# Optimization experiments

Hardware: AMD Instinct MI355X
Metric: run time of the kernel (lower is better)

## Reference

```python
import jax, jax.numpy as jnp
import numpy as np

DIM = 1536; FFN = 8960; NH = 12; HD = DIM // NH
B = 1; Fg, Hg, Wg = 8, 20, 20; L = Fg * Hg * Wg; L2 = 512
EPS = 1e-6; MAXLEN = 1024


def _rope_tables():
    # Wan rope_params: per-axis inverse-frequency tables, concatenated [t|h|w]
    c = HD // 2; c0 = c - 2 * (c // 3); c1 = c // 3
    def ang(dp):
        inv = 1.0 / (10000.0 ** (np.arange(0, dp, 2, dtype=np.float64) / dp))
        return np.outer(np.arange(MAXLEN, dtype=np.float64), inv)
    a = np.concatenate([ang(2 * c0), ang(2 * c1), ang(2 * c1)], axis=1)  # [1024, c]
    return np.cos(a).astype(np.float32), np.sin(a).astype(np.float32)


def setup_inputs() -> dict:
    key = jax.random.key(0)
    ks = jax.random.split(key, 32); it = iter(range(32))
    def rnd(shape, scale=0.02):
        return jax.random.normal(ks[next(it)], shape, dtype=jnp.float32) * scale
    cos, sin = _rope_tables()
    inp = {
        'x': rnd((B, L, DIM), 1.0),
        'e': rnd((B, 6, DIM), 1.0),
        'context': rnd((B, L2, DIM), 1.0),
        'freqs_cos': jnp.asarray(cos), 'freqs_sin': jnp.asarray(sin),
        'modulation': rnd((1, 6, DIM), DIM ** -0.5),
    }
    for p in ['sa', 'ca']:
        for nm in ['q', 'k', 'v', 'o']:
            inp[p + '_' + nm + 'w'] = rnd((DIM, DIM))
            inp[p + '_' + nm + 'b'] = jnp.zeros((DIM,), jnp.float32)
        inp[p + '_nq'] = jnp.ones((DIM,), jnp.float32)
        inp[p + '_nk'] = jnp.ones((DIM,), jnp.float32)
    inp['n3_w'] = jnp.ones((DIM,), jnp.float32); inp['n3_b'] = jnp.zeros((DIM,), jnp.float32)
    inp['ffn_w1'] = rnd((DIM, FFN)); inp['ffn_b1'] = jnp.zeros((FFN,), jnp.float32)
    inp['ffn_w2'] = rnd((FFN, DIM)); inp['ffn_b2'] = jnp.zeros((DIM,), jnp.float32)
    inp['grid_f'] = Fg; inp['grid_h'] = Hg; inp['grid_w'] = Wg
    return inp


def _layer_norm(x, w=None, b=None):
    mu = x.mean(-1, keepdims=True)
    var = jnp.mean((x - mu) ** 2, -1, keepdims=True)
    y = (x - mu) * jax.lax.rsqrt(var + EPS)
    return y * w + b if w is not None else y


def _rms(x, w):
    return x * jax.lax.rsqrt(jnp.mean(x * x, -1, keepdims=True) + EPS) * w


def _rope(xq, cos, sin, f, h, w):
    # xq: [B, L, n, d]; complex rotation per (t,h,w) axis with split freq dims
    b, s, n, d = xq.shape
    c = d // 2; c0 = c - 2 * (c // 3); c1 = c // 3
    def grid(tab):
        t = jnp.broadcast_to(tab[:f, None, None, :c0], (f, h, w, c0))
        hh = jnp.broadcast_to(tab[None, :h, None, c0:c0 + c1], (f, h, w, c1))
        ww = jnp.broadcast_to(tab[None, None, :w, c0 + c1:c0 + 2 * c1], (f, h, w, c1))
        return jnp.concatenate([t, hh, ww], -1).reshape(f * h * w, c)
    gc = grid(cos)[None, :, None, :]  # [1, L, 1, c]
    gs = grid(sin)[None, :, None, :]
    xr = xq.reshape(b, s, n, c, 2)
    xre, xim = xr[..., 0], xr[..., 1]
    return jnp.stack([xre * gc - xim * gs, xre * gs + xim * gc], -1).reshape(b, s, n, d)


def _attn(q, k, v):
    scores = jnp.einsum('bqnd,bknd->bnqk', q, k) * (q.shape[-1] ** -0.5)
    p = jax.nn.softmax(scores, -1)
    return jnp.einsum('bnqk,bknd->bqnd', p, v)


def reference(x, e, context, freqs_cos, freqs_sin, modulation,
              sa_qw, sa_qb, sa_kw, sa_kb, sa_vw, sa_vb, sa_ow, sa_ob, sa_nq, sa_nk,
              ca_qw, ca_qb, ca_kw, ca_kb, ca_vw, ca_vb, ca_ow, ca_ob, ca_nq, ca_nk,
              n3_w, n3_b, ffn_w1, ffn_b1, ffn_w2, ffn_b2,
              grid_f, grid_h, grid_w):
    b, s, _ = x.shape; n, d = NH, HD
    em = modulation + e  # [B, 6, C]
    e0, e1, e2, e3, e4, e5 = (em[:, i:i + 1] for i in range(6))
    # self-attention with adaLN modulation
    xs = _layer_norm(x) * (1 + e1) + e0
    q = _rms(xs @ sa_qw + sa_qb, sa_nq).reshape(b, s, n, d)
    k = _rms(xs @ sa_kw + sa_kb, sa_nk).reshape(b, s, n, d)
    v = (xs @ sa_vw + sa_vb).reshape(b, s, n, d)
    q = _rope(q, freqs_cos, freqs_sin, grid_f, grid_h, grid_w)
    k = _rope(k, freqs_cos, freqs_sin, grid_f, grid_h, grid_w)
    y = _attn(q, k, v).reshape(b, s, -1) @ sa_ow + sa_ob
    x = x + y * e2
    # cross-attention on norm3(x)
    xc = _layer_norm(x, n3_w, n3_b)
    s2 = context.shape[1]
    cq = _rms(xc @ ca_qw + ca_qb, ca_nq).reshape(b, s, n, d)
    ck = _rms(context @ ca_kw + ca_kb, ca_nk).reshape(b, s2, n, d)
    cv = (context @ ca_vw + ca_vb).reshape(b, s2, n, d)
    x = x + (_attn(cq, ck, cv).reshape(b, s, -1) @ ca_ow + ca_ob)
    # FFN with adaLN modulation
    xf = _layer_norm(x) * (1 + e4) + e3
    y = jax.nn.gelu(xf @ ffn_w1 + ffn_b1, approximate=True) @ ffn_w2 + ffn_b2
    return x + y * e5
```

## Files before the change

### kernel.cpp

```cpp
#include <hip/hip_runtime.h>

#define DIM 1536
#define NH 12
#define HD 128
#define LQ 3200
#define LKV 512
#define FFN 8960

typedef __attribute__((ext_vector_type(8))) short bf16x8;
typedef __attribute__((ext_vector_type(4))) float f32x4;
typedef __attribute__((ext_vector_type(4))) unsigned short u16x4;

__device__ inline unsigned short f2b(float f){
  union { float f; unsigned u; } x; x.f = f;
  unsigned r = (x.u + 0x7FFFu + ((x.u >> 16) & 1u)) >> 16;
  return (unsigned short)r;
}
__device__ inline float b2f(unsigned short u){
  union { unsigned u; float f; } x; x.u = ((unsigned)u) << 16; return x.f;
}
__device__ inline unsigned pack2(float a, float b){
  return (unsigned)f2b(a) | ((unsigned)f2b(b) << 16);
}
__device__ inline f32x4 mfma16(bf16x8 a, bf16x8 b, f32x4 c){
  return __builtin_amdgcn_mfma_f32_16x16x32_bf16(a, b, c, 0, 0, 0);
}
__device__ inline void gload_lds16(const unsigned short* g, unsigned short* l){
  __builtin_amdgcn_global_load_lds((const __attribute__((address_space(1))) unsigned int*)g,
                                   (__attribute__((address_space(3))) unsigned int*)l, 16, 0, 0);
}
__device__ inline int xcd_swizzle(int orig, int nwg){
  int q = nwg >> 3, r = nwg & 7;
  int xcd = orig & 7, off = orig >> 3;
  return (xcd < r ? xcd*(q+1) : r*(q+1) + (xcd-r)*q) + off;
}


__global__ void add_vec(const float* __restrict__ a, const float* __restrict__ b,
                        float* __restrict__ o, int n){
  int i = blockIdx.x*256 + threadIdx.x;
  if (i < n) o[i] = a[i] + b[i];
}

__global__ void convert_bf16(const float* __restrict__ a, unsigned short* __restrict__ o, int n){
  int i = blockIdx.x*256 + threadIdx.x;
  if (i < n) o[i] = f2b(a[i]);
}

__global__ void concat3(const float* __restrict__ a, const float* __restrict__ b,
                        const float* __restrict__ c, float* __restrict__ o, int n){
  int i = blockIdx.x*256 + threadIdx.x;
  if (i < n) o[i] = a[i];
  else if (i < 2*n) o[i] = b[i - n];
  else if (i < 3*n) o[i] = c[i - 2*n];
}

__global__ void transpose_conv(const float* __restrict__ src, unsigned short* __restrict__ dst,
                               int K, int N){
  __shared__ float tile[32][33];
  int n0 = blockIdx.x*32, k0 = blockIdx.y*32;
  int tx = threadIdx.x, ty = threadIdx.y;
  #pragma unroll
  for (int i = 0; i < 4; i++)
    tile[ty + 8*i][tx] = src[(size_t)(k0 + ty + 8*i)*N + n0 + tx];
  __syncthreads();
  #pragma unroll
  for (int i = 0; i < 4; i++)
    dst[(size_t)(n0 + ty + 8*i)*K + k0 + tx] = f2b(tile[tx][ty + 8*i]);
}

__global__ __launch_bounds__(256) void ln_mod_kernel(const float* __restrict__ x,
    const float* __restrict__ mulv, const float* __restrict__ addv, int one_plus,
    unsigned short* __restrict__ out){
  int row = blockIdx.x;
  const float* xr = x + (size_t)row * DIM;
  int tid = threadIdx.x;
  float v[6]; float s = 0.f, ss = 0.f;
  #pragma unroll
  for (int i = 0; i < 6; i++){ v[i] = xr[tid + i*256]; s += v[i]; ss += v[i]*v[i]; }
  #pragma unroll
  for (int m = 1; m < 64; m <<= 1){ s += __shfl_xor(s, m, 64); ss += __shfl_xor(ss, m, 64); }
  __shared__ float bs[4], bss[4];
  int w = tid >> 6;
  if ((tid & 63) == 0){ bs[w] = s; bss[w] = ss; }
  __syncthreads();
  s = bs[0]+bs[1]+bs[2]+bs[3]; ss = bss[0]+bss[1]+bss[2]+bss[3];
  float mu  = s * (1.f/DIM);
  float var = ss * (1.f/DIM) - mu*mu;
  float inv = rsqrtf(var + 1e-6f);
  unsigned short* orow = out + (size_t)row*DIM;
  #pragma unroll
  for (int i = 0; i < 6; i++){
    int c = tid + i*256;
    float g = one_plus ? (1.f + mulv[c]) : mulv[c];
    orow[c] = f2b((v[i]-mu)*inv*g + addv[c]);
  }
}

__global__ __launch_bounds__(256) void reduce_ln_kernel(const float* P0, const float* P1,
    const float* bias, const float* resid, const float* svec, float* out_x,
    const float* mulv, const float* addv, int one_plus, unsigned short* out_ln){
  int row = blockIdx.x;
  size_t base = (size_t)row * DIM;
  int tid = threadIdx.x;
  float v[6]; float s = 0.f, ss = 0.f;
  #pragma unroll
  for (int i = 0; i < 6; i++){
    int c = tid + i*256;
    float sv = svec ? svec[c] : 1.f;
    float y = resid[base + c] + (P0[base + c] + P1[base + c] + bias[c])*sv;
    out_x[base + c] = y;
    v[i] = y; s += y; ss += y*y;
  }
  #pragma unroll
  for (int m = 1; m < 64; m <<= 1){ s += __shfl_xor(s, m, 64); ss += __shfl_xor(ss, m, 64); }
  __shared__ float bs[4], bss[4];
  int w = tid >> 6;
  if ((tid & 63) == 0){ bs[w] = s; bss[w] = ss; }
  __syncthreads();
  s = bs[0]+bs[1]+bs[2]+bs[3]; ss = bss[0]+bss[1]+bss[2]+bss[3];
  float mu  = s * (1.f/DIM);
  float var = ss * (1.f/DIM) - mu*mu;
  float inv = rsqrtf(var + 1e-6f);
  unsigned short* orow = out_ln + base;
  #pragma unroll
  for (int i = 0; i < 6; i++){
    int c = tid + i*256;
    float g = one_plus ? (1.f + mulv[c]) : mulv[c];
    orow[c] = f2b((v[i]-mu)*inv*g + addv[c]);
  }
}

__global__ __launch_bounds__(256) void reduce_rms_kernel(const float* __restrict__ P0,
    const float* __restrict__ P1, const float* __restrict__ bias,
    const float* __restrict__ nw, unsigned short* __restrict__ out){
  int row = blockIdx.x;
  size_t base = (size_t)row * DIM;
  int tid = threadIdx.x;
  float v[6]; float ss = 0.f;
  #pragma unroll
  for (int i = 0; i < 6; i++){
    int c = tid + i*256;
    float y = P0[base + c] + P1[base + c] + bias[c];
    v[i] = y; ss += y*y;
  }
  #pragma unroll
  for (int m = 1; m < 64; m <<= 1) ss += __shfl_xor(ss, m, 64);
  __shared__ float bss[4];
  if ((tid & 63) == 0) bss[tid >> 6] = ss;
  __syncthreads();
  ss = bss[0]+bss[1]+bss[2]+bss[3];
  float inv = rsqrtf(ss*(1.f/DIM) + 1e-6f);
  #pragma unroll
  for (int i = 0; i < 6; i++){
    int c = tid + i*256;
    out[base + c] = f2b(v[i]*inv*nw[c]);
  }
}

__global__ __launch_bounds__(256) void rms_rope_b16(unsigned short* __restrict__ buf, int ld,
    const float* __restrict__ nw, const float* __restrict__ ct, const float* __restrict__ st,
    int do_rope){
  int row = blockIdx.x;
  unsigned short* xr = buf + (size_t)row*ld;
  int tid = threadIdx.x;
  float ss = 0.f; float v[6];
  #pragma unroll
  for (int i = 0; i < 6; i++){ v[i] = b2f(xr[tid + i*256]); ss += v[i]*v[i]; }
  #pragma unroll
  for (int m = 1; m < 64; m <<= 1) ss += __shfl_xor(ss, m, 64);
  __shared__ float bss[4];
  if ((tid & 63) == 0) bss[tid >> 6] = ss;
  __syncthreads();
  ss = bss[0]+bss[1]+bss[2]+bss[3];
  float inv = rsqrtf(ss*(1.f/DIM) + 1e-6f);
  if (!do_rope){
    #pragma unroll
    for (int i = 0; i < 6; i++){ int c = tid + i*256; xr[c] = f2b(v[i]*inv*nw[c]); }
  } else {
    int f = row/400, hp = (row/20)%20, wp = row%20;
    for (int p = tid; p < 768; p += 256){
      int hh = p >> 6, j = p & 63;
      int pos = (j < 22) ? f : ((j < 43) ? hp : wp);
      float c_ = ct[pos*64 + j], s_ = st[pos*64 + j];
      int base = hh*HD + 2*j;
      float xre = b2f(xr[base])   * inv * nw[base];
      float xim = b2f(xr[base+1]) * inv * nw[base+1];
      xr[base]   = f2b(xre*c_ - xim*s_);
      xr[base+1] = f2b(xre*s_ + xim*c_);
    }
  }
}

__global__ __launch_bounds__(256) void packvt_kernel(const unsigned short* __restrict__ pre, int ld,
    unsigned short* __restrict__ VT, int ntok){
  int h = blockIdx.y; int t0 = blockIdx.x*64;
  __shared__ unsigned short tile[128][72];
  int tid = threadIdx.x;
  int d = tid & 127, tl = tid >> 7;
  #pragma unroll 4
  for (int i = 0; i < 32; i++){
    int tok = t0 + tl + 2*i;
    tile[d][tl + 2*i] = pre[(size_t)tok*ld + h*HD + d];
  }
  __syncthreads();
  int dd = tid >> 6, tl2 = tid & 63;
  #pragma unroll 4
  for (int i = 0; i < 32; i++){
    int d2 = dd + 4*i;
    VT[((size_t)h*HD + d2)*ntok + t0 + tl2] = tile[d2][tl2];
  }
}

__global__ void reduce_f32(const float* P0, const float* P1,
    const float* bias, const float* resid,
    const float* svec, float* out, int total4){
  int i = blockIdx.x*256 + threadIdx.x;
  if (i >= total4) return;
  int col = (i*4) % DIM;
  float4 p0 = ((const float4*)P0)[i];
  float4 p1 = ((const float4*)P1)[i];
  float4 rs = ((const float4*)resid)[i];
  float4 o;
  float s0 = svec ? svec[col]   : 1.f;
  float s1 = svec ? svec[col+1] : 1.f;
  float s2 = svec ? svec[col+2] : 1.f;
  float s3 = svec ? svec[col+3] : 1.f;
  o.x = rs.x + (p0.x + p1.x + bias[col])*s0;
  o.y = rs.y + (p0.y + p1.y + bias[col+1])*s1;
  o.z = rs.z + (p0.z + p1.z + bias[col+2])*s2;
  o.w = rs.w + (p0.w + p1.w + bias[col+3])*s3;
  ((float4*)out)[i] = o;
}

__global__ __launch_bounds__(256) void gemm128_kernel(const unsigned short* __restrict__ A,
    const unsigned short* __restrict__ WT, const float* __restrict__ bias,
    int M, int N, int ldA, int ksize, int ep,
    float* __restrict__ outf0, float* __restrict__ outf1, unsigned short* __restrict__ outb){
  __shared__ unsigned short As[2][128*32];
  __shared__ unsigned short Bs[2][128*32];
  int t = threadIdx.x;
  int wv = t >> 6, lane = t & 63;
  int lr = lane & 15, lk = lane >> 4;
  int gx = gridDim.x;
  int nwg = gx * gridDim.y;
  int wg = xcd_swizzle(blockIdx.y*gx + blockIdx.x, nwg);
  int m0 = (wg % gx)*128, n0 = (wg / gx)*128;
  int kbeg = blockIdx.z*ksize;
  int wm = (wv >> 1)*64, wn = (wv & 1)*64;
  f32x4 z = {0.f,0.f,0.f,0.f};
  f32x4 acc[4][4];
  #pragma unroll
  for (int i = 0; i < 4; i++)
    #pragma unroll
    for (int j = 0; j < 4; j++) acc[i][j] = z;

  int srow = t >> 2;
  int sslot = (t & 3) ^ (srow & 3);
  const unsigned short* Ap0 = A  + (size_t)(m0 + srow)*ldA + kbeg + sslot*8;
  const unsigned short* Ap1 = A  + (size_t)(m0 + 64 + srow)*ldA + kbeg + sslot*8;
  const unsigned short* Bp0 = WT + (size_t)(n0 + srow)*ldA + kbeg + sslot*8;
  const unsigned short* Bp1 = WT + (size_t)(n0 + 64 + srow)*ldA + kbeg + sslot*8;
  int slA = (lk ^ (lr & 3))*8;

  int nk = ksize >> 5;
  gload_lds16(Ap0, &As[0][wv*512]);
  gload_lds16(Ap1, &As[0][2048 + wv*512]);
  gload_lds16(Bp0, &Bs[0][wv*512]);
  gload_lds16(Bp1, &Bs[0][2048 + wv*512]);
  asm volatile("s_waitcnt vmcnt(0)" ::: "memory");
  __syncthreads();

  for (int tt = 0; tt < nk; ++tt){
    int cur = tt & 1;
    if (tt + 1 < nk){
      int kn = (tt + 1) << 5;
      gload_lds16(Ap0 + kn, &As[cur^1][wv*512]);
      gload_lds16(Ap1 + kn, &As[cur^1][2048 + wv*512]);
      gload_lds16(Bp0 + kn, &Bs[cur^1][wv*512]);
      gload_lds16(Bp1 + kn, &Bs[cur^1][2048 + wv*512]);
    }
    bf16x8 af[4], bfr[4];
    #pragma unroll
    for (int i = 0; i < 4; i++){
      af[i]  = *(const bf16x8*)&As[cur][(wm + i*16 + lr)*32 + slA];
      bfr[i] = *(const bf16x8*)&Bs[cur][(wn + i*16 + lr)*32 + slA];
    }
    #pragma unroll
    for (int i = 0; i < 4; i++)
      #pragma unroll
      for (int j = 0; j < 4; j++)
        acc[i][j] = mfma16(af[i], bfr[j], acc[i][j]);
    asm volatile("s_waitcnt vmcnt(0)" ::: "memory");
    __syncthreads();
  }

  float* pdst = blockIdx.z ? outf1 : outf0;
  #pragma unroll
  for (int i = 0; i < 4; i++)
    #pragma unroll
    for (int j = 0; j < 4; j++)
      #pragma unroll
      for (int r = 0; r < 4; r++){
        int row = m0 + wm + i*16 + lk*4 + r;
        int col = n0 + wn + j*16 + lr;
        size_t idx = (size_t)row*N + col;
        if (ep == 4){
          pdst[idx] = acc[i][j][r];
        } else if (ep == 3){
          outb[idx] = f2b(acc[i][j][r] + bias[col]);
        } else {
          float vv = acc[i][j][r] + bias[col];
          float u = 0.79788456080286535588f*(vv + 0.044715f*vv*vv*vv);
          u = fminf(fmaxf(u, -20.f), 20.f);
          float e2u = __expf(2.f*u);
          float th = (e2u - 1.f)/(e2u + 1.f);
          outb[idx] = f2b(0.5f*vv*(1.f+th));
        }
      }
}

__global__ __launch_bounds__(256, 3) void attn_kernel(const unsigned short* __restrict__ Q, int ldQ,
    const unsigned short* __restrict__ Kg, int ldK, const unsigned short* __restrict__ VT,
    unsigned short* __restrict__ O, int nkv, int vlen){
  __shared__ unsigned short Kls[64*128];
  __shared__ unsigned short Vls[128*64];
  __shared__ unsigned short Pls[4][16][80];
  int gx = gridDim.x;
  int wg = xcd_swizzle(blockIdx.y*gx + blockIdx.x, gx*gridDim.y);
  int bq = wg % gx, h = wg / gx;
  int tid = threadIdx.x;
  int wv = tid >> 6, lane = tid & 63;
  int lr = lane & 15, lk = lane >> 4;
  int q0 = bq*64 + wv*16;

  bf16x8 qf[4];
  const unsigned short* qp = Q + (size_t)(q0 + lr)*ldQ + h*HD + lk*8;
  #pragma unroll
  for (int kk = 0; kk < 4; kk++) qf[kk] = *(const bf16x8*)(qp + kk*32);

  f32x4 z = {0.f,0.f,0.f,0.f};
  f32x4 acc[8];
  #pragma unroll
  for (int d = 0; d < 8; d++) acc[d] = z;
  float mrun = -1e30f, lrun = 0.f;
  const float sc = 0.08838834764831845f;
  int swz = (lr & 7) << 4;

  for (int kt = 0; kt < nkv; kt += 64){
    __syncthreads();
    #pragma unroll
    for (int j = 0; j < 4; j++){
      int row = wv*16 + j*4 + (lane >> 4);
      int cb  = ((lane & 15)*16) ^ ((row & 7) << 4);
      gload_lds16(Kg + (size_t)(kt + row)*ldK + h*HD + (cb >> 1),
                  &Kls[(wv*16 + j*4)*128]);
    }
    #pragma unroll
    for (int j = 0; j < 4; j++){
      int d  = wv*32 + j*8 + (lane >> 3);
      int cb = ((lane & 7)*16) ^ ((d & 7) << 4);
      gload_lds16(VT + ((size_t)h*HD + d)*vlen + kt + (cb >> 1),
                  &Vls[(wv*32 + j*8)*64]);
    }
    asm volatile("s_waitcnt vmcnt(0)" ::: "memory");
    __syncthreads();

    f32x4 s[4];
    #pragma unroll
    for (int t4 = 0; t4 < 4; t4++) s[t4] = z;
    #pragma unroll
    for (int t4 = 0; t4 < 4; t4++){
      #pragma unroll
      for (int kk = 0; kk < 4; kk++){
        bf16x8 kf = *(const bf16x8*)&Kls[(t4*16 + lr)*128 + (((kk*64 + lk*16) ^ swz) >> 1)];
        s[t4] = mfma16(kf, qf[kk], s[t4]);
      }
    }

    float vv[4][4]; float pmax = -1e30f;
    #pragma unroll
    for (int t4 = 0; t4 < 4; t4++)
      #pragma unroll
      for (int r = 0; r < 4; r++){
        float xv = s[t4][r]*sc; vv[t4][r] = xv; pmax = fmaxf(pmax, xv);
      }
    pmax = fmaxf(pmax, __shfl_xor(pmax, 16, 64));
    pmax = fmaxf(pmax, __shfl_xor(pmax, 32, 64));
    float mn = fmaxf(mrun, pmax);
    float cr = __expf(mrun - mn);
    mrun = mn;
    float rs = 0.f;
    #pragma unroll
    for (int t4 = 0; t4 < 4; t4++)
      #pragma unroll
      for (int r = 0; r < 4; r++){
        float pv = __expf(vv[t4][r] - mn); vv[t4][r] = pv; rs += pv;
      }
    rs += __shfl_xor(rs, 16, 64);
    rs += __shfl_xor(rs, 32, 64);
    lrun = lrun*cr + rs;
    #pragma unroll
    for (int d = 0; d < 8; d++) acc[d] *= cr;

    #pragma unroll
    for (int t4 = 0; t4 < 4; t4++){
      *(unsigned*)&Pls[wv][lr][t4*16 + lk*4]     = pack2(vv[t4][0], vv[t4][1]);
      *(unsigned*)&Pls[wv][lr][t4*16 + lk*4 + 2] = pack2(vv[t4][2], vv[t4][3]);
    }
    bf16x8 pb0 = *(const bf16x8*)&Pls[wv][lr][lk*8];
    bf16x8 pb1 = *(const bf16x8*)&Pls[wv][lr][32 + lk*8];

    #pragma unroll
    for (int db = 0; db < 8; db++){
      bf16x8 vf0 = *(const bf16x8*)&Vls[(db*16 + lr)*64 + (((lk*16) ^ swz) >> 1)];
      acc[db] = mfma16(vf0, pb0, acc[db]);
      bf16x8 vf1 = *(const bf16x8*)&Vls[(db*16 + lr)*64 + (((64 + lk*16) ^ swz) >> 1)];
      acc[db] = mfma16(vf1, pb1, acc[db]);
    }
  }

  float inv = 1.f/lrun;
  unsigned short* op = O + (size_t)(q0 + lr)*DIM + h*HD + lk*4;
  #pragma unroll
  for (int db = 0; db < 8; db++){
    u16x4 ov;
    ov[0] = f2b(acc[db][0]*inv); ov[1] = f2b(acc[db][1]*inv);
    ov[2] = f2b(acc[db][2]*inv); ov[3] = f2b(acc[db][3]*inv);
    *(u16x4*)(op + db*16) = ov;
  }
}


extern "C" void kernel_launch(void* const* d_in, const int* in_sizes, int n_in,
                              void* d_out, int out_size, void* d_ws, size_t ws_size,
                              hipStream_t stream){
  const float* x    = (const float*)d_in[0];
  const float* e    = (const float*)d_in[1];
  const float* ctx  = (const float*)d_in[2];
  const float* fcos = (const float*)d_in[3];
  const float* fsin = (const float*)d_in[4];
  const float* modu = (const float*)d_in[5];
  const float* sa_qw = (const float*)d_in[6];  const float* sa_qb = (const float*)d_in[7];
  const float* sa_kw = (const float*)d_in[8];  const float* sa_kb = (const float*)d_in[9];
  const float* sa_vw = (const float*)d_in[10]; const float* sa_vb = (const float*)d_in[11];
  const float* sa_ow = (const float*)d_in[12]; const float* sa_ob = (const float*)d_in[13];
  const float* sa_nq = (const float*)d_in[14]; const float* sa_nk = (const float*)d_in[15];
  const float* ca_qw = (const float*)d_in[16]; const float* ca_qb = (const float*)d_in[17];
  const float* ca_kw = (const float*)d_in[18]; const float* ca_kb = (const float*)d_in[19];
  const float* ca_vw = (const float*)d_in[20]; const float* ca_vb = (const float*)d_in[21];
  const float* ca_ow = (const float*)d_in[22]; const float* ca_ob = (const float*)d_in[23];
  const float* ca_nq = (const float*)d_in[24]; const float* ca_nk = (const float*)d_in[25];
  const float* n3w = (const float*)d_in[26]; const float* n3b = (const float*)d_in[27];
  const float* fw1 = (const float*)d_in[28]; const float* fb1 = (const float*)d_in[29];
  const float* fw2 = (const float*)d_in[30]; const float* fb2 = (const float*)d_in[31];

  char* p = (char*)d_ws;
  auto alloc = [&](size_t bytes){ void* r = (void*)p; p += (bytes + 255) & ~(size_t)255; return r; };
  unsigned short* wt[8];
  for (int i = 0; i < 8; i++) wt[i] = (unsigned short*)alloc((size_t)DIM*DIM*2);
  unsigned short* wtf1 = (unsigned short*)alloc((size_t)FFN*DIM*2);
  unsigned short* wtf2 = (unsigned short*)alloc((size_t)DIM*FFN*2);
  float* em     = (float*)alloc(6*DIM*4);
  float* qkvb   = (float*)alloc(3*DIM*4);
  float* ckvb   = (float*)alloc(2*DIM*4);
  unsigned short* nbuf = (unsigned short*)alloc((size_t)LQ*DIM*2);
  unsigned short* qkv16 = (unsigned short*)alloc((size_t)LQ*3*DIM*2);
  unsigned short* VTb   = (unsigned short*)alloc((size_t)LQ*DIM*2);
  unsigned short* Qb    = (unsigned short*)alloc((size_t)LQ*DIM*2);
  unsigned short* Ob    = (unsigned short*)alloc((size_t)LQ*DIM*2);
  float* x1 = (float*)alloc((size_t)LQ*DIM*4);
  unsigned short* ctxb   = (unsigned short*)alloc((size_t)LKV*DIM*2);
  unsigned short* cakv16 = (unsigned short*)alloc((size_t)LKV*2*DIM*2);

  float* P0   = (float*)d_out;
  float* P1a  = (float*)qkv16;
  float* P1f  = (float*)wtf1;
  unsigned short* hbuf = qkv16;
  const int TOT4 = LQ*DIM/4;

  add_vec<<<36, 256, 0, stream>>>(modu, e, em, 6*DIM);
  concat3<<<18, 256, 0, stream>>>(sa_qb, sa_kb, sa_vb, qkvb, DIM);
  concat3<<<12, 256, 0, stream>>>(ca_kb, ca_vb, ca_vb, ckvb, DIM);
  const float* wsrc[8] = {sa_qw, sa_kw, sa_vw, sa_ow, ca_qw, ca_kw, ca_vw, ca_ow};
  for (int i = 0; i < 8; i++)
    transpose_conv<<<dim3(48,48), dim3(32,8), 0, stream>>>(wsrc[i], wt[i], DIM, DIM);
  transpose_conv<<<dim3(280,48), dim3(32,8), 0, stream>>>(fw1, wtf1, DIM, FFN);
  transpose_conv<<<dim3(48,280), dim3(32,8), 0, stream>>>(fw2, wtf2, FFN, DIM);
  convert_bf16<<<(LKV*DIM)/256, 256, 0, stream>>>(ctx, ctxb, LKV*DIM);

  ln_mod_kernel<<<LQ, 256, 0, stream>>>(x, em + DIM, em, 1, nbuf);
  gemm128_kernel<<<dim3(25,36,1), 256, 0, stream>>>(nbuf, wt[0], qkvb, LQ, 3*DIM, DIM, DIM, 3,
                                                    nullptr, nullptr, qkv16);
  rms_rope_b16<<<LQ, 256, 0, stream>>>(qkv16,        3*DIM, sa_nq, fcos, fsin, 1);
  rms_rope_b16<<<LQ, 256, 0, stream>>>(qkv16 + DIM,  3*DIM, sa_nk, fcos, fsin, 1);
  packvt_kernel<<<dim3(50,12), 256, 0, stream>>>(qkv16 + 2*DIM, 3*DIM, VTb, LQ);
  attn_kernel<<<dim3(50,12), 256, 0, stream>>>(qkv16, 3*DIM, qkv16 + DIM, 3*DIM, VTb, Ob, LQ, LQ);
  gemm128_kernel<<<dim3(25,12,2), 256, 0, stream>>>(Ob, wt[3], nullptr, LQ, DIM, DIM, DIM/2, 4,
                                                    P0, P1a, nullptr);
  reduce_ln_kernel<<<LQ, 256, 0, stream>>>(P0, P1a, sa_ob, x, em + 2*DIM, x1,
                                           n3w, n3b, 0, nbuf);

  gemm128_kernel<<<dim3(25,12,2), 256, 0, stream>>>(nbuf, wt[4], nullptr, LQ, DIM, DIM, DIM/2, 4,
                                                    P0, P1a, nullptr);
  reduce_rms_kernel<<<LQ, 256, 0, stream>>>(P0, P1a, ca_qb, ca_nq, Qb);
  gemm128_kernel<<<dim3(4,24,1), 256, 0, stream>>>(ctxb, wt[5], ckvb, LKV, 2*DIM, DIM, DIM, 3,
                                                   nullptr, nullptr, cakv16);
  rms_rope_b16<<<LKV, 256, 0, stream>>>(cakv16, 2*DIM, ca_nk, fcos, fsin, 0);
  packvt_kernel<<<dim3(8,12), 256, 0, stream>>>(cakv16 + DIM, 2*DIM, VTb, LKV);
  attn_kernel<<<dim3(50,12), 256, 0, stream>>>(Qb, DIM, cakv16, 2*DIM, VTb, Ob, LKV, LKV);
  gemm128_kernel<<<dim3(25,12,2), 256, 0, stream>>>(Ob, wt[7], nullptr, LQ, DIM, DIM, DIM/2, 4,
                                                    P0, P1a, nullptr);
  reduce_ln_kernel<<<LQ, 256, 0, stream>>>(P0, P1a, ca_ob, x1, nullptr, x1,
                                           em + 4*DIM, em + 3*DIM, 1, nbuf);

  gemm128_kernel<<<dim3(25,70,1), 256, 0, stream>>>(nbuf, wtf1, fb1, LQ, FFN, DIM, DIM, 2,
                                                    nullptr, nullptr, hbuf);
  gemm128_kernel<<<dim3(25,12,2), 256, 0, stream>>>(hbuf, wtf2, nullptr, LQ, DIM, FFN, FFN/2, 4,
                                                    P0, P1f, nullptr);
  reduce_f32<<<(TOT4+255)/256, 256, 0, stream>>>(P0, P1f, fb2, x1, em + 5*DIM, (float*)d_out, TOT4);
}
```

Before: 867.5 us.

## Add 256x256-tile 8-wave GEMM kernel for QKV and FFN-up projections

Introduces a new GEMM kernel with 256x256 output tiles, 512 threads and double-buffered LDS loads via global_load_lds, with swizzled LDS layout and setprio around MFMA blocks. It replaces the 128-tile GEMM for the fused QKV projection and the FFN up-projection with GELU. Larger tiles raise arithmetic intensity and cut global traffic per FLOP. In exchange, M=3200 is not a multiple of 256, so the last tile reads past the end of nbuf, which is padded by 128 rows and moved ahead of x1 to stay in bounds; the grid also shrinks to fewer, larger workgroups, which may leave CUs underused.

```diff
diff --git a/kernel.cpp b/kernel.cpp
--- a/kernel.cpp
+++ b/kernel.cpp
@@ -33,6 +33,13 @@
   int q = nwg >> 3, r = nwg & 7;
   int xcd = orig & 7, off = orig >> 3;
   return (xcd < r ? xcd*(q+1) : r*(q+1) + (xcd-r)*q) + off;
+}
+__device__ inline float gelu_f(float vv){
+  float u = 0.79788456080286535588f*(vv + 0.044715f*vv*vv*vv);
+  u = fminf(fmaxf(u, -20.f), 20.f);
+  float e2u = __expf(2.f*u);
+  float th = (e2u - 1.f)/(e2u + 1.f);
+  return 0.5f*vv*(1.f+th);
 }
 
 
@@ -310,12 +317,114 @@
         } else if (ep == 3){
           outb[idx] = f2b(acc[i][j][r] + bias[col]);
         } else {
-          float vv = acc[i][j][r] + bias[col];
-          float u = 0.79788456080286535588f*(vv + 0.044715f*vv*vv*vv);
-          u = fminf(fmaxf(u, -20.f), 20.f);
-          float e2u = __expf(2.f*u);
-          float th = (e2u - 1.f)/(e2u + 1.f);
-          outb[idx] = f2b(0.5f*vv*(1.f+th));
+          outb[idx] = f2b(gelu_f(acc[i][j][r] + bias[col]));
+        }
+      }
+}
+
+__global__ __launch_bounds__(512, 2) void gemm256_kernel(const unsigned short* __restrict__ A,
+    const unsigned short* __restrict__ WT, const float* __restrict__ bias,
+    int M, int N, int ldA, int K, int ep, unsigned short* __restrict__ outb){
+  __shared__ unsigned short As[2][256*64];
+  __shared__ unsigned short Bs[2][256*64];
+  int t = threadIdx.x;
+  int wv = t >> 6, lane = t & 63;
+  int lr = lane & 15, lk = lane >> 4;
+  int wr = wv >> 2, wc = wv & 3;
+  int gx = gridDim.x;
+  int wg = xcd_swizzle(blockIdx.y*gx + blockIdx.x, gx*gridDim.y);
+  int m0 = (wg % gx)*256, n0 = (wg / gx)*256;
+
+  f32x4 z = {0.f,0.f,0.f,0.f};
+  f32x4 acc[8][4];
+  #pragma unroll
+  for (int i = 0; i < 8; i++)
+    #pragma unroll
+    for (int j = 0; j < 4; j++) acc[i][j] = z;
+
+  int srow_in = lane >> 3;
+  int pslot = lane & 7;
+  int rA = wr*128 + lr;
+  int rB = wc*64 + lr;
+  int swz = lr & 7;
+
+  int nk = K >> 6;
+  #pragma unroll
+  for (int h = 0; h < 2; h++)
+    #pragma unroll
+    for (int pp = 0; pp < 2; pp++){
+      int rbase = h*128 + pp*64 + wv*8;
+      int row = rbase + srow_in;
+      int gs = pslot ^ (row & 7);
+      gload_lds16(A  + (size_t)(m0 + row)*ldA + gs*8, &As[0][rbase*64]);
+      gload_lds16(WT + (size_t)(n0 + row)*ldA + gs*8, &Bs[0][rbase*64]);
+    }
+
+  for (int tt = 0; tt < nk; ++tt){
+    int cur = tt & 1;
+    if (tt + 1 < nk){
+      int kt = (tt + 1) << 6;
+      #pragma unroll
+      for (int h = 0; h < 2; h++)
+        #pragma unroll
+        for (int pp = 0; pp < 2; pp++){
+          int rbase = h*128 + pp*64 + wv*8;
+          int row = rbase + srow_in;
+          int gs = pslot ^ (row & 7);
+          gload_lds16(A  + (size_t)(m0 + row)*ldA + kt + gs*8, &As[cur^1][rbase*64]);
+          gload_lds16(WT + (size_t)(n0 + row)*ldA + kt + gs*8, &Bs[cur^1][rbase*64]);
+        }
+      asm volatile("s_waitcnt vmcnt(8)" ::: "memory");
+    } else {
+      asm volatile("s_waitcnt vmcnt(0)" ::: "memory");
+    }
+    __builtin_amdgcn_s_barrier();
+    __builtin_amdgcn_sched_barrier(0);
+
+    bf16x8 bfr[4][2];
+    #pragma unroll
+    for (int q = 0; q < 4; q++){
+      if (q == 0){
+        #pragma unroll
+        for (int j = 0; j < 4; j++)
+          #pragma unroll
+          for (int kk = 0; kk < 2; kk++)
+            bfr[j][kk] = *(const bf16x8*)&Bs[cur][(rB + j*16)*64 + (((kk*4 + lk) ^ swz))*8];
+      }
+      bf16x8 af[2][2];
+      #pragma unroll
+      for (int mi2 = 0; mi2 < 2; mi2++)
+        #pragma unroll
+        for (int kk = 0; kk < 2; kk++)
+          af[mi2][kk] = *(const bf16x8*)&As[cur][(rA + (2*q + mi2)*16)*64 + (((kk*4 + lk) ^ swz))*8];
+      __builtin_amdgcn_s_barrier();
+      asm volatile("s_waitcnt lgkmcnt(0)" ::: "memory");
+      __builtin_amdgcn_sched_barrier(0);
+      __builtin_amdgcn_s_setprio(1);
+      #pragma unroll
+      for (int mi2 = 0; mi2 < 2; mi2++)
+        #pragma unroll
+        for (int j = 0; j < 4; j++)
+          #pragma unroll
+          for (int kk = 0; kk < 2; kk++)
+            acc[2*q + mi2][j] = mfma16(af[mi2][kk], bfr[j][kk], acc[2*q + mi2][j]);
+      __builtin_amdgcn_s_setprio(0);
+      __builtin_amdgcn_s_barrier();
+    }
+  }
+
+  #pragma unroll
+  for (int mi = 0; mi < 8; mi++)
+    #pragma unroll
+    for (int j = 0; j < 4; j++)
+      #pragma unroll
+      for (int rr = 0; rr < 4; rr++){
+        int row = m0 + wr*128 + mi*16 + lk*4 + rr;
+        if (row < M){
+          int col = n0 + wc*64 + j*16 + lr;
+          size_t idx = (size_t)row*N + col;
+          float vv = acc[mi][j][rr] + bias[col];
+          outb[idx] = (ep == 3) ? f2b(vv) : f2b(gelu_f(vv));
         }
       }
 }
@@ -464,14 +573,14 @@
   float* em     = (float*)alloc(6*DIM*4);
   float* qkvb   = (float*)alloc(3*DIM*4);
   float* ckvb   = (float*)alloc(2*DIM*4);
-  unsigned short* nbuf = (unsigned short*)alloc((size_t)LQ*DIM*2);
+  unsigned short* nbuf = (unsigned short*)alloc((size_t)(LQ+128)*DIM*2);
   unsigned short* qkv16 = (unsigned short*)alloc((size_t)LQ*3*DIM*2);
   unsigned short* VTb   = (unsigned short*)alloc((size_t)LQ*DIM*2);
   unsigned short* Qb    = (unsigned short*)alloc((size_t)LQ*DIM*2);
   unsigned short* Ob    = (unsigned short*)alloc((size_t)LQ*DIM*2);
-  float* x1 = (float*)alloc((size_t)LQ*DIM*4);
   unsigned short* ctxb   = (unsigned short*)alloc((size_t)LKV*DIM*2);
   unsigned short* cakv16 = (unsigned short*)alloc((size_t)LKV*2*DIM*2);
+  float* x1 = (float*)alloc((size_t)LQ*DIM*4);
 
   float* P0   = (float*)d_out;
   float* P1a  = (float*)qkv16;
@@ -490,8 +599,7 @@
   convert_bf16<<<(LKV*DIM)/256, 256, 0, stream>>>(ctx, ctxb, LKV*DIM);
 
   ln_mod_kernel<<<LQ, 256, 0, stream>>>(x, em + DIM, em, 1, nbuf);
-  gemm128_kernel<<<dim3(25,36,1), 256, 0, stream>>>(nbuf, wt[0], qkvb, LQ, 3*DIM, DIM, DIM, 3,
-                                                    nullptr, nullptr, qkv16);
+  gemm256_kernel<<<dim3(13,18), 512, 0, stream>>>(nbuf, wt[0], qkvb, LQ, 3*DIM, DIM, DIM, 3, qkv16);
   rms_rope_b16<<<LQ, 256, 0, stream>>>(qkv16,        3*DIM, sa_nq, fcos, fsin, 1);
   rms_rope_b16<<<LQ, 256, 0, stream>>>(qkv16 + DIM,  3*DIM, sa_nk, fcos, fsin, 1);
   packvt_kernel<<<dim3(50,12), 256, 0, stream>>>(qkv16 + 2*DIM, 3*DIM, VTb, LQ);
@@ -514,8 +622,7 @@
   reduce_ln_kernel<<<LQ, 256, 0, stream>>>(P0, P1a, ca_ob, x1, nullptr, x1,
                                            em + 4*DIM, em + 3*DIM, 1, nbuf);
 
-  gemm128_kernel<<<dim3(25,70,1), 256, 0, stream>>>(nbuf, wtf1, fb1, LQ, FFN, DIM, DIM, 2,
-                                                    nullptr, nullptr, hbuf);
+  gemm256_kernel<<<dim3(13,35), 512, 0, stream>>>(nbuf, wtf1, fb1, LQ, FFN, DIM, DIM, 2, hbuf);
   gemm128_kernel<<<dim3(25,12,2), 256, 0, stream>>>(hbuf, wtf2, nullptr, LQ, DIM, FFN, FFN/2, 4,
                                                     P0, P1f, nullptr);
   reduce_f32<<<(TOT4+255)/256, 256, 0, stream>>>(P0, P1f, fb2, x1, em + 5*DIM, (float*)d_out, TOT4);
```

After: 875.7 us. Within noise of the previous version (+0.9%).

## Use 8-wave 512-thread GEMM blocks and fuse Q/K RMS-rope launches

Applied to the files above, without the earlier changes.

The 128x128 GEMM tile is now split across 8 waves instead of 4. Each wave owns a 32x64 sub-tile with half the accumulators, and each thread issues half as many global-to-LDS loads. The goal is more resident waves to hide memory and MFMA latency, at the cost of fewer MFMAs per LDS fragment read. The two self-attention RMS+rope launches are merged into one 2D-grid kernel, and the no-rope path becomes its own kernel. GELU is moved into a helper function.

```diff
diff --git a/kernel.cpp b/kernel.cpp
--- a/kernel.cpp
+++ b/kernel.cpp
@@ -34,6 +34,13 @@
   int xcd = orig & 7, off = orig >> 3;
   return (xcd < r ? xcd*(q+1) : r*(q+1) + (xcd-r)*q) + off;
 }
+__device__ inline float gelu_f(float vv){
+  float u = 0.79788456080286535588f*(vv + 0.044715f*vv*vv*vv);
+  u = fminf(fmaxf(u, -20.f), 20.f);
+  float e2u = __expf(2.f*u);
+  float th = (e2u - 1.f)/(e2u + 1.f);
+  return 0.5f*vv*(1.f+th);
+}
 
 
 __global__ void add_vec(const float* __restrict__ a, const float* __restrict__ b,
@@ -158,11 +165,13 @@
   }
 }
 
-__global__ __launch_bounds__(256) void rms_rope_b16(unsigned short* __restrict__ buf, int ld,
-    const float* __restrict__ nw, const float* __restrict__ ct, const float* __restrict__ st,
-    int do_rope){
+__global__ __launch_bounds__(256) void rms_rope_qk(unsigned short* __restrict__ buf,
+    const float* __restrict__ nwq, const float* __restrict__ nwk,
+    const float* __restrict__ ct, const float* __restrict__ st){
   int row = blockIdx.x;
-  unsigned short* xr = buf + (size_t)row*ld;
+  int sl = blockIdx.y;
+  const float* nw = sl ? nwk : nwq;
+  unsigned short* xr = buf + (size_t)row*(3*DIM) + sl*DIM;
   int tid = threadIdx.x;
   float ss = 0.f; float v[6];
   #pragma unroll
@@ -174,22 +183,36 @@
   __syncthreads();
   ss = bss[0]+bss[1]+bss[2]+bss[3];
   float inv = rsqrtf(ss*(1.f/DIM) + 1e-6f);
-  if (!do_rope){
-    #pragma unroll
-    for (int i = 0; i < 6; i++){ int c = tid + i*256; xr[c] = f2b(v[i]*inv*nw[c]); }
-  } else {
-    int f = row/400, hp = (row/20)%20, wp = row%20;
-    for (int p = tid; p < 768; p += 256){
-      int hh = p >> 6, j = p & 63;
-      int pos = (j < 22) ? f : ((j < 43) ? hp : wp);
-      float c_ = ct[pos*64 + j], s_ = st[pos*64 + j];
-      int base = hh*HD + 2*j;
-      float xre = b2f(xr[base])   * inv * nw[base];
-      float xim = b2f(xr[base+1]) * inv * nw[base+1];
-      xr[base]   = f2b(xre*c_ - xim*s_);
-      xr[base+1] = f2b(xre*s_ + xim*c_);
-    }
-  }
+  int f = row/400, hp = (row/20)%20, wp = row%20;
+  for (int p = tid; p < 768; p += 256){
+    int hh = p >> 6, j = p & 63;
+    int pos = (j < 22) ? f : ((j < 43) ? hp : wp);
+    float c_ = ct[pos*64 + j], s_ = st[pos*64 + j];
+    int base = hh*HD + 2*j;
+    float xre = b2f(xr[base])   * inv * nw[base];
+    float xim = b2f(xr[base+1]) * inv * nw[base+1];
+    xr[base]   = f2b(xre*c_ - xim*s_);
+    xr[base+1] = f2b(xre*s_ + xim*c_);
+  }
+}
+
+__global__ __launch_bounds__(256) void rms_rope_b16(unsigned short* __restrict__ buf, int ld,
+    const float* __restrict__ nw){
+  int row = blockIdx.x;
+  unsigned short* xr = buf + (size_t)row*ld;
+  int tid = threadIdx.x;
+  float ss = 0.f; float v[6];
+  #pragma unroll
+  for (int i = 0; i < 6; i++){ v[i] = b2f(xr[tid + i*256]); ss += v[i]*v[i]; }
+  #pragma unroll
+  for (int m = 1; m < 64; m <<= 1) ss += __shfl_xor(ss, m, 64);
+  __shared__ float bss[4];
+  if ((tid & 63) == 0) bss[tid >> 6] = ss;
+  __syncthreads();
+  ss = bss[0]+bss[1]+bss[2]+bss[3];
+  float inv = rsqrtf(ss*(1.f/DIM) + 1e-6f);
+  #pragma unroll
+  for (int i = 0; i < 6; i++){ int c = tid + i*256; xr[c] = f2b(v[i]*inv*nw[c]); }
 }
 
 __global__ __launch_bounds__(256) void packvt_kernel(const unsigned short* __restrict__ pre, int ld,
@@ -233,7 +256,7 @@
   ((float4*)out)[i] = o;
 }
 
-__global__ __launch_bounds__(256) void gemm128_kernel(const unsigned short* __restrict__ A,
+__global__ __launch_bounds__(512, 4) void gemm128_kernel(const unsigned short* __restrict__ A,
     const unsigned short* __restrict__ WT, const float* __restrict__ bias,
     int M, int N, int ldA, int ksize, int ep,
     float* __restrict__ outf0, float* __restrict__ outf1, unsigned short* __restrict__ outb){
@@ -247,27 +270,23 @@
   int wg = xcd_swizzle(blockIdx.y*gx + blockIdx.x, nwg);
   int m0 = (wg % gx)*128, n0 = (wg / gx)*128;
   int kbeg = blockIdx.z*ksize;
-  int wm = (wv >> 1)*64, wn = (wv & 1)*64;
+  int wm = (wv >> 1)*32, wn = (wv & 1)*64;
   f32x4 z = {0.f,0.f,0.f,0.f};
-  f32x4 acc[4][4];
-  #pragma unroll
-  for (int i = 0; i < 4; i++)
+  f32x4 acc[2][4];
+  #pragma unroll
+  for (int i = 0; i < 2; i++)
     #pragma unroll
     for (int j = 0; j < 4; j++) acc[i][j] = z;
 
   int srow = t >> 2;
   int sslot = (t & 3) ^ (srow & 3);
   const unsigned short* Ap0 = A  + (size_t)(m0 + srow)*ldA + kbeg + sslot*8;
-  const unsigned short* Ap1 = A  + (size_t)(m0 + 64 + srow)*ldA + kbeg + sslot*8;
   const unsigned short* Bp0 = WT + (size_t)(n0 + srow)*ldA + kbeg + sslot*8;
-  const unsigned short* Bp1 = WT + (size_t)(n0 + 64 + srow)*ldA + kbeg + sslot*8;
   int slA = (lk ^ (lr & 3))*8;
 
   int nk = ksize >> 5;
   gload_lds16(Ap0, &As[0][wv*512]);
-  gload_lds16(Ap1, &As[0][2048 + wv*512]);
   gload_lds16(Bp0, &Bs[0][wv*512]);
-  gload_lds16(Bp1, &Bs[0][2048 + wv*512]);
   asm volatile("s_waitcnt vmcnt(0)" ::: "memory");
   __syncthreads();
 
@@ -276,18 +295,17 @@
     if (tt + 1 < nk){
       int kn = (tt + 1) << 5;
       gload_lds16(Ap0 + kn, &As[cur^1][wv*512]);
-      gload_lds16(Ap1 + kn, &As[cur^1][2048 + wv*512]);
       gload_lds16(Bp0 + kn, &Bs[cur^1][wv*512]);
-      gload_lds16(Bp1 + kn, &Bs[cur^1][2048 + wv*512]);
     }
-    bf16x8 af[4], bfr[4];
-    #pragma unroll
-    for (int i = 0; i < 4; i++){
+    bf16x8 af[2], bfr[4];
+    #pragma unroll
+    for (int i = 0; i < 2; i++)
       af[i]  = *(const bf16x8*)&As[cur][(wm + i*16 + lr)*32 + slA];
-      bfr[i] = *(const bf16x8*)&Bs[cur][(wn + i*16 + lr)*32 + slA];
-    }
-    #pragma unroll
-    for (int i = 0; i < 4; i++)
+    #pragma unroll
+    for (int j = 0; j < 4; j++)
+      bfr[j] = *(const bf16x8*)&Bs[cur][(wn + j*16 + lr)*32 + slA];
+    #pragma unroll
+    for (int i = 0; i < 2; i++)
       #pragma unroll
       for (int j = 0; j < 4; j++)
         acc[i][j] = mfma16(af[i], bfr[j], acc[i][j]);
@@ -297,7 +315,7 @@
 
   float* pdst = blockIdx.z ? outf1 : outf0;
   #pragma unroll
-  for (int i = 0; i < 4; i++)
+  for (int i = 0; i < 2; i++)
     #pragma unroll
     for (int j = 0; j < 4; j++)
       #pragma unroll
@@ -310,12 +328,7 @@
         } else if (ep == 3){
           outb[idx] = f2b(acc[i][j][r] + bias[col]);
         } else {
-          float vv = acc[i][j][r] + bias[col];
-          float u = 0.79788456080286535588f*(vv + 0.044715f*vv*vv*vv);
-          u = fminf(fmaxf(u, -20.f), 20.f);
-          float e2u = __expf(2.f*u);
-          float th = (e2u - 1.f)/(e2u + 1.f);
-          outb[idx] = f2b(0.5f*vv*(1.f+th));
+          outb[idx] = f2b(gelu_f(acc[i][j][r] + bias[col]));
         }
       }
 }
@@ -490,33 +503,32 @@
   convert_bf16<<<(LKV*DIM)/256, 256, 0, stream>>>(ctx, ctxb, LKV*DIM);
 
   ln_mod_kernel<<<LQ, 256, 0, stream>>>(x, em + DIM, em, 1, nbuf);
-  gemm128_kernel<<<dim3(25,36,1), 256, 0, stream>>>(nbuf, wt[0], qkvb, LQ, 3*DIM, DIM, DIM, 3,
+  gemm128_kernel<<<dim3(25,36,1), 512, 0, stream>>>(nbuf, wt[0], qkvb, LQ, 3*DIM, DIM, DIM, 3,
                                                     nullptr, nullptr, qkv16);
-  rms_rope_b16<<<LQ, 256, 0, stream>>>(qkv16,        3*DIM, sa_nq, fcos, fsin, 1);
-  rms_rope_b16<<<LQ, 256, 0, stream>>>(qkv16 + DIM,  3*DIM, sa_nk, fcos, fsin, 1);
+  rms_rope_qk<<<dim3(LQ,2), 256, 0, stream>>>(qkv16, sa_nq, sa_nk, fcos, fsin);
   packvt_kernel<<<dim3(50,12), 256, 0, stream>>>(qkv16 + 2*DIM, 3*DIM, VTb, LQ);
   attn_kernel<<<dim3(50,12), 256, 0, stream>>>(qkv16, 3*DIM, qkv16 + DIM, 3*DIM, VTb, Ob, LQ, LQ);
-  gemm128_kernel<<<dim3(25,12,2), 256, 0, stream>>>(Ob, wt[3], nullptr, LQ, DIM, DIM, DIM/2, 4,
+  gemm128_kernel<<<dim3(25,12,2), 512, 0, stream>>>(Ob, wt[3], nullptr, LQ, DIM, DIM, DIM/2, 4,
                                                     P0, P1a, nullptr);
   reduce_ln_kernel<<<LQ, 256, 0, stream>>>(P0, P1a, sa_ob, x, em + 2*DIM, x1,
                                            n3w, n3b, 0, nbuf);
 
-  gemm128_kernel<<<dim3(25,12,2), 256, 0, stream>>>(nbuf, wt[4], nullptr, LQ, DIM, DIM, DIM/2, 4,
+  gemm128_kernel<<<dim3(25,12,2), 512, 0, stream>>>(nbuf, wt[4], nullptr, LQ, DIM, DIM, DIM/2, 4,
                                                     P0, P1a, nullptr);
   reduce_rms_kernel<<<LQ, 256, 0, stream>>>(P0, P1a, ca_qb, ca_nq, Qb);
-  gemm128_kernel<<<dim3(4,24,1), 256, 0, stream>>>(ctxb, wt[5], ckvb, LKV, 2*DIM, DIM, DIM, 3,
+  gemm128_kernel<<<dim3(4,24,1), 512, 0, stream>>>(ctxb, wt[5], ckvb, LKV, 2*DIM, DIM, DIM, 3,
                                                    nullptr, nullptr, cakv16);
-  rms_rope_b16<<<LKV, 256, 0, stream>>>(cakv16, 2*DIM, ca_nk, fcos, fsin, 0);
+  rms_rope_b16<<<LKV, 256, 0, stream>>>(cakv16, 2*DIM, ca_nk);
   packvt_kernel<<<dim3(8,12), 256, 0, stream>>>(cakv16 + DIM, 2*DIM, VTb, LKV);
   attn_kernel<<<dim3(50,12), 256, 0, stream>>>(Qb, DIM, cakv16, 2*DIM, VTb, Ob, LKV, LKV);
-  gemm128_kernel<<<dim3(25,12,2), 256, 0, stream>>>(Ob, wt[7], nullptr, LQ, DIM, DIM, DIM/2, 4,
+  gemm128_kernel<<<dim3(25,12,2), 512, 0, stream>>>(Ob, wt[7], nullptr, LQ, DIM, DIM, DIM/2, 4,
                                                     P0, P1a, nullptr);
   reduce_ln_kernel<<<LQ, 256, 0, stream>>>(P0, P1a, ca_ob, x1, nullptr, x1,
                                            em + 4*DIM, em + 3*DIM, 1, nbuf);
 
-  gemm128_kernel<<<dim3(25,70,1), 256, 0, stream>>>(nbuf, wtf1, fb1, LQ, FFN, DIM, DIM, 2,
+  gemm128_kernel<<<dim3(25,70,1), 512, 0, stream>>>(nbuf, wtf1, fb1, LQ, FFN, DIM, DIM, 2,
                                                     nullptr, nullptr, hbuf);
-  gemm128_kernel<<<dim3(25,12,2), 256, 0, stream>>>(hbuf, wtf2, nullptr, LQ, DIM, FFN, FFN/2, 4,
+  gemm128_kernel<<<dim3(25,12,2), 512, 0, stream>>>(hbuf, wtf2, nullptr, LQ, DIM, FFN, FFN/2, 4,
                                                     P0, P1f, nullptr);
   reduce_f32<<<(TOT4+255)/256, 256, 0, stream>>>(P0, P1f, fb2, x1, em + 5*DIM, (float*)d_out, TOT4);
 }
```

Result: faster. 829.1 us (-4.4%).
